# Performance work log

Hardware: AMD Instinct MI355X
Metric: run time of the kernel (lower is better)

Reference implementation:

```python
import jax, jax.numpy as jnp
import numpy as np

IN_FEATURES = 4096
OUT_FEATURES = 4096
NNZ = 1677722
TOKENS = 8192


def setup_inputs() -> dict:
    key = jax.random.key(0)
    k_x, k_val, k_row, k_col, k_b = jax.random.split(key, 5)
    x = jax.random.normal(k_x, (TOKENS, IN_FEATURES), dtype=jnp.float32)
    values = jax.random.normal(k_val, (NNZ,), dtype=jnp.float32)
    row_ids = jax.random.randint(k_row, (NNZ,), 0, OUT_FEATURES, dtype=jnp.int32)
    col_ids = jax.random.randint(k_col, (NNZ,), 0, IN_FEATURES, dtype=jnp.int32)
    bias = jax.random.normal(k_b, (OUT_FEATURES,), dtype=jnp.float32)
    return {"x": x, "values": values, "row_ids": row_ids, "col_ids": col_ids, "bias": bias}


def reference(x, values, row_ids, col_ids, bias):
    # F.linear(input, W_sparse, bias) == x @ W^T + bias where W is the
    # (out_features, in_features) sparse weight. Materialize W from its
    # nonzeros with a scatter-add (duplicate coords sum, matching sparse semantics),
    # then use a single dense matmul.
    out_f = bias.shape[0]
    in_f = x.shape[-1]
    W = jnp.zeros((out_f, in_f), dtype=x.dtype).at[row_ids, col_ids].add(values)
    return x @ W.T + bias
```

## Files before the change

### kernel.cpp

```cpp
#include <hip/hip_runtime.h>
#include <hip/hip_bf16.h>
#include <stdint.h>

#define IN_F 4096
#define OUT_F 4096
#define NTOK 8192

typedef __attribute__((ext_vector_type(8))) __bf16 bf16x8;
typedef __attribute__((ext_vector_type(4))) float f32x4;

__device__ __forceinline__ unsigned short f2bf(float f) {
    unsigned u = __float_as_uint(f);
    u += 0x7fffu + ((u >> 16) & 1u);
    return (unsigned short)(u >> 16);
}

__global__ void scatter_kernel(const float* __restrict__ vals,
                               const int* __restrict__ rows,
                               const int* __restrict__ cols,
                               float* __restrict__ W, int nnz) {
    int i = blockIdx.x * blockDim.x + threadIdx.x;
    if (i < nnz) {
        atomicAdd(&W[(size_t)rows[i] * IN_F + cols[i]], vals[i]);
    }
}

__global__ void cvt_kernel(const float4* __restrict__ in, ushort4* __restrict__ out, int n4) {
    int stride = gridDim.x * blockDim.x;
    for (int i = blockIdx.x * blockDim.x + threadIdx.x; i < n4; i += stride) {
        float4 v = in[i];
        ushort4 o;
        o.x = f2bf(v.x); o.y = f2bf(v.y); o.z = f2bf(v.z); o.w = f2bf(v.w);
        out[i] = o;
    }
}

#define GLD_LDS16(gp, lp)                                              \
    __builtin_amdgcn_global_load_lds(                                  \
        (__attribute__((address_space(1))) void*)(void*)(gp),          \
        (__attribute__((address_space(3))) void*)(lp), 16, 0, 0)

__global__ __launch_bounds__(256, 2)
void gemm_bt_bias(const ushort* __restrict__ A,
                  const ushort* __restrict__ B,
                  const float* __restrict__ bias,
                  float* __restrict__ C) {
    constexpr int M = NTOK, N = OUT_F, K = IN_F;
    constexpr int TM = 128, TN = 128, BK = 64;

    __shared__ ushort As[TM * BK];
    __shared__ ushort Bs[TN * BK];

    const int tid  = threadIdx.x;
    const int lane = tid & 63;
    const int wid  = tid >> 6;

    const int nbx  = N / TN;
    const int bx   = blockIdx.x % nbx;
    const int by   = blockIdx.x / nbx;
    const int brow = by * TM;
    const int bcol = bx * TN;

    const int wr = wid >> 1, wc = wid & 1;

    f32x4 acc[4][4] = {};

    const int srow = wid * 8 + (lane >> 3);
    const int scol = (lane & 7) * 8;
    const ushort* aptr = A + (size_t)(brow + srow) * K + scol;
    const ushort* bptr = B + (size_t)(bcol + srow) * K + scol;

    for (int k0 = 0; k0 < K; k0 += BK) {
        __syncthreads();
#pragma unroll
        for (int r = 0; r < 4; ++r)
            GLD_LDS16(aptr + (size_t)(r * 32) * K + k0, &As[(r * 32 + wid * 8) * BK]);
#pragma unroll
        for (int r = 0; r < 4; ++r)
            GLD_LDS16(bptr + (size_t)(r * 32) * K + k0, &Bs[(r * 32 + wid * 8) * BK]);
        __syncthreads();

#pragma unroll
        for (int kk = 0; kk < BK; kk += 32) {
            bf16x8 af[4], bg[4];
#pragma unroll
            for (int m = 0; m < 4; ++m)
                af[m] = *(const bf16x8*)&As[(wr * 64 + m * 16 + (lane & 15)) * BK + kk + (lane >> 4) * 8];
#pragma unroll
            for (int n = 0; n < 4; ++n)
                bg[n] = *(const bf16x8*)&Bs[(wc * 64 + n * 16 + (lane & 15)) * BK + kk + (lane >> 4) * 8];
#pragma unroll
            for (int m = 0; m < 4; ++m)
#pragma unroll
                for (int n = 0; n < 4; ++n)
                    acc[m][n] = __builtin_amdgcn_mfma_f32_16x16x32_bf16(af[m], bg[n], acc[m][n], 0, 0, 0);
        }
    }

    const int crow0 = brow + wr * 64;
    const int ccol0 = bcol + wc * 64;
#pragma unroll
    for (int n = 0; n < 4; ++n) {
        const int col = ccol0 + n * 16 + (lane & 15);
        const float bv = bias[col];
#pragma unroll
        for (int m = 0; m < 4; ++m) {
            const int row0 = crow0 + m * 16 + (lane >> 4) * 4;
#pragma unroll
            for (int j = 0; j < 4; ++j)
                C[(size_t)(row0 + j) * N + col] = acc[m][n][j] + bv;
        }
    }
}

extern "C" void kernel_launch(void* const* d_in, const int* in_sizes, int n_in,
                              void* d_out, int out_size, void* d_ws, size_t ws_size,
                              hipStream_t stream) {
    const float* x    = (const float*)d_in[0];
    const float* vals = (const float*)d_in[1];
    const int*   rows = (const int*)d_in[2];
    const int*   cols = (const int*)d_in[3];
    const float* bias = (const float*)d_in[4];
    float* out = (float*)d_out;
    const int nnz = in_sizes[1];

    char* ws = (char*)d_ws;
    float*  Wf = (float*)ws;
    ushort* Wb = (ushort*)(ws + (size_t)64 * 1024 * 1024);
    ushort* Xb = (ushort*)(ws + (size_t)96 * 1024 * 1024);

    hipMemsetAsync(Wf, 0, (size_t)OUT_F * IN_F * sizeof(float), stream);
    scatter_kernel<<<(nnz + 255) / 256, 256, 0, stream>>>(vals, rows, cols, Wf, nnz);
    cvt_kernel<<<2048, 256, 0, stream>>>((const float4*)Wf, (ushort4*)Wb, OUT_F * IN_F / 4);
    cvt_kernel<<<2048, 256, 0, stream>>>((const float4*)x,  (ushort4*)Xb, NTOK * IN_F / 4);
    gemm_bt_bias<<<dim3((NTOK / 128) * (OUT_F / 128)), 256, 0, stream>>>(Xb, Wb, bias, out);
}
```

Measured before the change: 609.5 us.

## Rebuild bf16 GEMM with 256x256 tiles and 4-stage swizzled LDS pipeline

The GEMM moves from 128x128 tiles with 256 threads and a single-buffered LDS loop to 256x256 tiles with 512 threads. Global-to-LDS loads run three k-steps ahead through a 4-buffer ring, gated by explicit vmcnt waits and one barrier per step. LDS addresses use an XOR swizzle, and block indices are remapped to improve L2 reuse. The two fp32-to-bf16 conversion launches are merged into one kernel. The aim is to hide memory latency and raise MFMA utilisation, at the cost of 128KB of dynamic LDS and higher register pressure, which limits occupancy to one block per CU.

```diff
diff --git a/kernel.cpp b/kernel.cpp
--- a/kernel.cpp
+++ b/kernel.cpp
@@ -20,18 +20,21 @@
                                const int* __restrict__ cols,
                                float* __restrict__ W, int nnz) {
     int i = blockIdx.x * blockDim.x + threadIdx.x;
-    if (i < nnz) {
-        atomicAdd(&W[(size_t)rows[i] * IN_F + cols[i]], vals[i]);
-    }
+    if (i < nnz) atomicAdd(&W[(size_t)rows[i] * IN_F + cols[i]], vals[i]);
 }
 
-__global__ void cvt_kernel(const float4* __restrict__ in, ushort4* __restrict__ out, int n4) {
+__global__ void cvt2_kernel(const float4* __restrict__ a, ushort4* __restrict__ oa, int na4,
+                            const float4* __restrict__ b, ushort4* __restrict__ ob, int nb4) {
     int stride = gridDim.x * blockDim.x;
-    for (int i = blockIdx.x * blockDim.x + threadIdx.x; i < n4; i += stride) {
-        float4 v = in[i];
+    int tot = na4 + nb4;
+    for (int i = blockIdx.x * blockDim.x + threadIdx.x; i < tot; i += stride) {
+        const float4* src; ushort4* dst; int j;
+        if (i < na4) { src = a; dst = oa; j = i; }
+        else         { src = b; dst = ob; j = i - na4; }
+        float4 v = src[j];
         ushort4 o;
         o.x = f2bf(v.x); o.y = f2bf(v.y); o.z = f2bf(v.z); o.w = f2bf(v.w);
-        out[i] = o;
+        dst[j] = o;
     }
 }
 
@@ -40,75 +43,106 @@
         (__attribute__((address_space(1))) void*)(void*)(gp),          \
         (__attribute__((address_space(3))) void*)(lp), 16, 0, 0)
 
-__global__ __launch_bounds__(256, 2)
+#define STAGE(tt) do {                                                 \
+    const int _b = ((tt) & 3) * 16384;                                 \
+    const size_t _k = (size_t)(tt) * 32;                               \
+    GLD_LDS16(A0 + _k, &lds[_b + ldst0]);                              \
+    GLD_LDS16(A1 + _k, &lds[_b + ldst1]);                              \
+    GLD_LDS16(B0 + _k, &lds[_b + 8192 + ldst0]);                       \
+    GLD_LDS16(B1 + _k, &lds[_b + 8192 + ldst1]);                       \
+} while (0)
+
+template<int VM>
+__device__ __forceinline__ void kiter(int t,
+        const ushort* __restrict__ A0, const ushort* __restrict__ A1,
+        const ushort* __restrict__ B0, const ushort* __restrict__ B1,
+        ushort* lds, int ldst0, int ldst1,
+        const int (&aoff)[8], const int (&boff)[4], f32x4 (&acc)[8][4]) {
+    if constexpr (VM == 8)      asm volatile("s_waitcnt vmcnt(8)" ::: "memory");
+    else if constexpr (VM == 4) asm volatile("s_waitcnt vmcnt(4)" ::: "memory");
+    else                        asm volatile("s_waitcnt vmcnt(0)" ::: "memory");
+    __builtin_amdgcn_s_barrier();
+    if (t + 3 < IN_F / 32) STAGE(t + 3);
+    const int bb = (t & 3) * 16384;
+    bf16x8 af[8], bg[4];
+#pragma unroll
+    for (int m = 0; m < 8; ++m) af[m] = *(const bf16x8*)&lds[bb + aoff[m]];
+#pragma unroll
+    for (int n = 0; n < 4; ++n) bg[n] = *(const bf16x8*)&lds[bb + 8192 + boff[n]];
+    __builtin_amdgcn_s_setprio(1);
+#pragma unroll
+    for (int m = 0; m < 8; ++m)
+#pragma unroll
+        for (int n = 0; n < 4; ++n)
+            acc[m][n] = __builtin_amdgcn_mfma_f32_16x16x32_bf16(af[m], bg[n], acc[m][n], 0, 0, 0);
+    __builtin_amdgcn_s_setprio(0);
+}
+
+__global__ __launch_bounds__(512, 2)
 void gemm_bt_bias(const ushort* __restrict__ A,
                   const ushort* __restrict__ B,
                   const float* __restrict__ bias,
                   float* __restrict__ C) {
-    constexpr int M = NTOK, N = OUT_F, K = IN_F;
-    constexpr int TM = 128, TN = 128, BK = 64;
+    constexpr int N = OUT_F, K = IN_F;
+    constexpr int NT = K / 32;
 
-    __shared__ ushort As[TM * BK];
-    __shared__ ushort Bs[TN * BK];
+    extern __shared__ ushort lds[];
 
     const int tid  = threadIdx.x;
     const int lane = tid & 63;
     const int wid  = tid >> 6;
 
-    const int nbx  = N / TN;
-    const int bx   = blockIdx.x % nbx;
-    const int by   = blockIdx.x / nbx;
-    const int brow = by * TM;
-    const int bcol = bx * TN;
+    const int bid = blockIdx.x;
+    const int nb  = (bid & 7) * 64 + (bid >> 3);
+    const int by = nb >> 4, bx = nb & 15;
+    const int brow = by * 256, bcol = bx * 256;
 
-    const int wr = wid >> 1, wc = wid & 1;
+    const int wr = wid >> 2, wc = wid & 3;
 
-    f32x4 acc[4][4] = {};
+    const int d0 = tid * 8, d1 = (512 + tid) * 8;
+    const int s0 = d0 ^ (((d0 >> 6) & 7) << 3);
+    const int s1 = d1 ^ (((d1 >> 6) & 7) << 3);
+    const ushort* A0 = A + (size_t)(brow + (s0 >> 5)) * K + (s0 & 31);
+    const ushort* A1 = A + (size_t)(brow + (s1 >> 5)) * K + (s1 & 31);
+    const ushort* B0 = B + (size_t)(bcol + (s0 >> 5)) * K + (s0 & 31);
+    const ushort* B1 = B + (size_t)(bcol + (s1 >> 5)) * K + (s1 & 31);
+    const int ldst0 = (wid * 64) * 8;
+    const int ldst1 = (512 + wid * 64) * 8;
 
-    const int srow = wid * 8 + (lane >> 3);
-    const int scol = (lane & 7) * 8;
-    const ushort* aptr = A + (size_t)(brow + srow) * K + scol;
-    const ushort* bptr = B + (size_t)(bcol + srow) * K + scol;
-
-    for (int k0 = 0; k0 < K; k0 += BK) {
-        __syncthreads();
+    const int fr = lane & 15, kq = (lane >> 4) * 8;
+    int aoff[8], boff[4];
 #pragma unroll
-        for (int r = 0; r < 4; ++r)
-            GLD_LDS16(aptr + (size_t)(r * 32) * K + k0, &As[(r * 32 + wid * 8) * BK]);
+    for (int m = 0; m < 8; ++m) {
+        int lin = (wr * 128 + m * 16 + fr) * 32 + kq;
+        aoff[m] = lin ^ (((lin >> 6) & 7) << 3);
+    }
 #pragma unroll
-        for (int r = 0; r < 4; ++r)
-            GLD_LDS16(bptr + (size_t)(r * 32) * K + k0, &Bs[(r * 32 + wid * 8) * BK]);
-        __syncthreads();
-
-#pragma unroll
-        for (int kk = 0; kk < BK; kk += 32) {
-            bf16x8 af[4], bg[4];
-#pragma unroll
-            for (int m = 0; m < 4; ++m)
-                af[m] = *(const bf16x8*)&As[(wr * 64 + m * 16 + (lane & 15)) * BK + kk + (lane >> 4) * 8];
-#pragma unroll
-            for (int n = 0; n < 4; ++n)
-                bg[n] = *(const bf16x8*)&Bs[(wc * 64 + n * 16 + (lane & 15)) * BK + kk + (lane >> 4) * 8];
-#pragma unroll
-            for (int m = 0; m < 4; ++m)
-#pragma unroll
-                for (int n = 0; n < 4; ++n)
-                    acc[m][n] = __builtin_amdgcn_mfma_f32_16x16x32_bf16(af[m], bg[n], acc[m][n], 0, 0, 0);
-        }
+    for (int n = 0; n < 4; ++n) {
+        int lin = (wc * 64 + n * 16 + fr) * 32 + kq;
+        boff[n] = lin ^ (((lin >> 6) & 7) << 3);
     }
 
-    const int crow0 = brow + wr * 64;
+    f32x4 acc[8][4] = {};
+
+    STAGE(0); STAGE(1); STAGE(2);
+
+    for (int t = 0; t < NT - 2; ++t)
+        kiter<8>(t, A0, A1, B0, B1, lds, ldst0, ldst1, aoff, boff, acc);
+    kiter<4>(NT - 2, A0, A1, B0, B1, lds, ldst0, ldst1, aoff, boff, acc);
+    kiter<0>(NT - 1, A0, A1, B0, B1, lds, ldst0, ldst1, aoff, boff, acc);
+
+    const int crow0 = brow + wr * 128;
     const int ccol0 = bcol + wc * 64;
 #pragma unroll
     for (int n = 0; n < 4; ++n) {
-        const int col = ccol0 + n * 16 + (lane & 15);
+        const int col = ccol0 + n * 16 + fr;
         const float bv = bias[col];
 #pragma unroll
-        for (int m = 0; m < 4; ++m) {
-            const int row0 = crow0 + m * 16 + (lane >> 4) * 4;
+        for (int m = 0; m < 8; ++m) {
+            const int r0 = crow0 + m * 16 + (lane >> 4) * 4;
 #pragma unroll
             for (int j = 0; j < 4; ++j)
-                C[(size_t)(row0 + j) * N + col] = acc[m][n][j] + bv;
+                C[(size_t)(r0 + j) * N + col] = acc[m][n][j] + bv;
         }
     }
 }
@@ -131,7 +165,7 @@
 
     hipMemsetAsync(Wf, 0, (size_t)OUT_F * IN_F * sizeof(float), stream);
     scatter_kernel<<<(nnz + 255) / 256, 256, 0, stream>>>(vals, rows, cols, Wf, nnz);
-    cvt_kernel<<<2048, 256, 0, stream>>>((const float4*)Wf, (ushort4*)Wb, OUT_F * IN_F / 4);
-    cvt_kernel<<<2048, 256, 0, stream>>>((const float4*)x,  (ushort4*)Xb, NTOK * IN_F / 4);
-    gemm_bt_bias<<<dim3((NTOK / 128) * (OUT_F / 128)), 256, 0, stream>>>(Xb, Wb, bias, out);
+    cvt2_kernel<<<4096, 256, 0, stream>>>((const float4*)Wf, (ushort4*)Wb, OUT_F * IN_F / 4,
+                                          (const float4*)x,  (ushort4*)Xb, NTOK * IN_F / 4);
+    gemm_bt_bias<<<dim3((NTOK / 256) * (OUT_F / 256)), 512, 131072, stream>>>(Xb, Wb, bias, out);
 }
```

Result: faster. 551.5 us (-9.5%).
